# Kernel tuning notes

Measured on AMD Instinct MI355X. Metric: run time of the kernel, lower is better.

The kernel has to match this reference:

```python
import jax, jax.numpy as jnp
import numpy as np
from jax import lax

N = 100000   # num_nodes
E = 1600000  # num_edges (avg degree 16)
F = 128      # num_features
H = 256      # hidden_channels
C = 64       # num_classes
K = 10       # propagation steps
ALPHA = 0.1
BETA = 0.5
THETA = 0.5
EPS = 1e-5   # BatchNorm eps


def setup_inputs() -> dict:
    key = jax.random.key(0)
    ks = jax.random.split(key, 16)
    x = jax.random.normal(ks[0], (N, F), dtype=jnp.float32)
    src = jax.random.randint(ks[1], (E,), 0, N, dtype=jnp.int32)
    dst = jax.random.randint(ks[2], (E,), 0, N, dtype=jnp.int32)
    # row-normalized adjacency weights so repeated A@z stays bounded
    deg = jax.ops.segment_sum(jnp.ones((E,), jnp.float32), dst, num_segments=N)
    w = (1.0 / jnp.maximum(deg, 1.0))[dst]
    # MLP params (Linear + BatchNorm per hidden layer)
    W1 = jax.random.normal(ks[3], (F, H), dtype=jnp.float32) * 0.05
    b1 = jnp.zeros((H,), jnp.float32)
    g1 = jnp.ones((H,), jnp.float32)
    be1 = jnp.zeros((H,), jnp.float32)
    W2 = jax.random.normal(ks[4], (H, H), dtype=jnp.float32) * 0.05
    b2 = jnp.zeros((H,), jnp.float32)
    g2 = jnp.ones((H,), jnp.float32)
    be2 = jnp.zeros((H,), jnp.float32)
    W3 = jax.random.normal(ks[5], (H, C), dtype=jnp.float32) * 0.05
    b3 = jnp.zeros((C,), jnp.float32)
    # lazy caches (warm-start memories); nonzero so the blend branch is taken
    z_sam = jax.random.normal(ks[6], (N, C), dtype=jnp.float32) * 0.1
    g_sam = jax.random.normal(ks[7], (N, C), dtype=jnp.float32) * 0.01
    return dict(x=x, src=src, dst=dst, w=w,
                W1=W1, b1=b1, g1=g1, be1=be1,
                W2=W2, b2=b2, g2=g2, be2=be2,
                W3=W3, b3=b3, z_sam=z_sam, g_sam=g_sam, size=N)


def _bn(h, gamma, beta):
    # BatchNorm1d in training mode: batch statistics over nodes
    mu = jnp.mean(h, axis=0)
    var = jnp.var(h, axis=0)
    return (h - mu) * jax.lax.rsqrt(var + EPS) * gamma + beta


def reference(x, src, dst, w, W1, b1, g1, be1, W2, b2, g2, be2, W3, b3,
              z_sam, g_sam, size):
    # MLP stack: Linear -> BN -> ReLU (dropout omitted: deterministic reference)
    h = jax.nn.relu(_bn(x @ W1 + b1, g1, be1))
    h = jax.nn.relu(_bn(h @ W2 + b2, g2, be2))
    logits = h @ W3 + b3  # [N, C]

    def spmm(z):
        # (A @ z)_i = sum_{j -> i} w_ij * z_j
        return jax.ops.segment_sum(z[src] * w[:, None], dst, num_segments=N)

    # Lazy_Prop.forward: warm-start blend, then K propagation steps
    use_x = jnp.all(z_sam[:size] == 0.0)
    z0 = jnp.where(use_x, logits, (1.0 - BETA) * z_sam + BETA * logits)
    z = lax.fori_loop(0, K, lambda i, z: (1.0 - ALPHA) * spmm(z) + ALPHA * logits, z0)
    return jax.nn.log_softmax(z, axis=1)
```

## Files before the change

kernel.cpp:

```cpp
#include <hip/hip_runtime.h>
#include <hip/hip_bf16.h>

#define NODES 100000
#define EDGES 1600000
#define FEAT  128
#define HID   256
#define CLS   64
#define KPROP 10
#define ALPHA_C 0.1f
#define BETA_C  0.5f
#define BN_EPS  1e-5f

typedef __attribute__((ext_vector_type(8))) short short8;
typedef __attribute__((ext_vector_type(4))) float f32x4;

static __device__ __forceinline__ unsigned short f2b(float f) {
    __hip_bfloat16 h = __float2bfloat16(f);
    return *(unsigned short*)&h;
}
static __device__ __forceinline__ float b2f(unsigned short u) {
    __hip_bfloat16 h;
    *(unsigned short*)&h = u;
    return __bfloat162float(h);
}
static __device__ __forceinline__ float asf(unsigned int u) {
    union { unsigned int u; float f; } c; c.u = u; return c.f;
}

__global__ void packwt_k(const float* __restrict__ W, unsigned short* __restrict__ Wt,
                         int K, int N)
{
    int i = blockIdx.x * 256 + threadIdx.x;
    if (i < K * N) {
        int k = i / N, n = i - k * N;
        Wt[(size_t)n * K + k] = f2b(W[i]);
    }
}

__global__ void xcvt_k(const float* __restrict__ x, unsigned short* __restrict__ xb)
{
    int i = blockIdx.x * 256 + threadIdx.x;
    if (i < NODES * FEAT / 8) {
        float4 a = ((const float4*)x)[2 * i];
        float4 b = ((const float4*)x)[2 * i + 1];
        short8 o;
        o[0] = (short)f2b(a.x); o[1] = (short)f2b(a.y);
        o[2] = (short)f2b(a.z); o[3] = (short)f2b(a.w);
        o[4] = (short)f2b(b.x); o[5] = (short)f2b(b.y);
        o[6] = (short)f2b(b.z); o[7] = (short)f2b(b.w);
        ((short8*)xb)[i] = o;
    }
}

__global__ __launch_bounds__(256, 2)
void gemm1_k(const unsigned short* __restrict__ xb, const unsigned short* __restrict__ Wt,
             const float* __restrict__ bias, unsigned short* __restrict__ h1,
             float* __restrict__ gsum, float* __restrict__ gsq,
             int M, int nchunks, int nblk)
{
    __shared__ unsigned short Blds[256 * FEAT];
    const int lane = threadIdx.x & 63;
    const int wv   = threadIdx.x >> 6;
    const int quad = lane >> 4;
    const int l16  = lane & 15;
    const int colbase = wv * 64;

    #pragma unroll
    for (int i0 = 0; i0 < 4096; i0 += 256) {
        int i  = i0 + threadIdx.x;
        int c  = i >> 4;
        int k8 = i & 15;
        short8 v = *(const short8*)(Wt + (size_t)c * FEAT + k8 * 8);
        int byte = c * 256 + ((k8 * 16) ^ ((c & 7) << 4));
        *(short8*)((char*)Blds + byte) = v;
    }
    __syncthreads();

    float bcol[4];
    #pragma unroll
    for (int ct = 0; ct < 4; ++ct) bcol[ct] = bias[colbase + ct * 16 + l16];
    float ps[4] = {0.f, 0.f, 0.f, 0.f};
    float pq[4] = {0.f, 0.f, 0.f, 0.f};

    short8 ah0[2][4], ah1[2][4];

#define LOAD1(AH, CHK)                                                         \
    if ((CHK) < nchunks) {                                                     \
        const int rb_ = (CHK) * 32;                                            \
        _Pragma("unroll")                                                      \
        for (int rt = 0; rt < 2; ++rt) {                                       \
            const int row_ = rb_ + rt * 16 + l16;                              \
            const bool ok_ = row_ < M;                                         \
            const unsigned short* ap_ = xb + (size_t)row_ * FEAT + quad * 8;   \
            _Pragma("unroll")                                                  \
            for (int ks = 0; ks < 4; ++ks)                                     \
                AH[rt][ks] = ok_ ? *(const short8*)(ap_ + ks * 32)             \
                                 : (short8){0, 0, 0, 0, 0, 0, 0, 0};           \
        }                                                                      \
    }

#define COMP1(AH, CHK)                                                         \
    {                                                                          \
        const int rb_ = (CHK) * 32;                                            \
        f32x4 acc[2][4];                                                       \
        _Pragma("unroll")                                                      \
        for (int i = 0; i < 2; ++i)                                            \
            _Pragma("unroll")                                                  \
            for (int j = 0; j < 4; ++j)                                        \
                acc[i][j] = (f32x4){0.f, 0.f, 0.f, 0.f};                       \
        _Pragma("unroll")                                                      \
        for (int ks = 0; ks < 4; ++ks) {                                       \
            _Pragma("unroll")                                                  \
            for (int ct = 0; ct < 4; ++ct) {                                   \
                const int col_ = colbase + ct * 16 + l16;                      \
                const int boff = col_ * 256                                    \
                               + ((ks * 64 + quad * 16) ^ ((col_ & 7) << 4));  \
                short8 bf = *(const short8*)((const char*)Blds + boff);        \
                acc[0][ct] = __builtin_amdgcn_mfma_f32_16x16x32_bf16(AH[0][ks], bf, acc[0][ct], 0, 0, 0); \
                acc[1][ct] = __builtin_amdgcn_mfma_f32_16x16x32_bf16(AH[1][ks], bf, acc[1][ct], 0, 0, 0); \
            }                                                                  \
        }                                                                      \
        _Pragma("unroll")                                                      \
        for (int ct = 0; ct < 4; ++ct) {                                       \
            const int col_ = colbase + ct * 16 + l16;                          \
            _Pragma("unroll")                                                  \
            for (int rt = 0; rt < 2; ++rt) {                                   \
                _Pragma("unroll")                                              \
                for (int r2 = 0; r2 < 4; ++r2) {                               \
                    const int row_ = rb_ + rt * 16 + quad * 4 + r2;            \
                    if (row_ < M) {                                            \
                        float vv = acc[rt][ct][r2] + bcol[ct];                 \
                        ps[ct] += vv; pq[ct] += vv * vv;                       \
                        h1[(size_t)row_ * HID + col_] = f2b(vv);               \
                    }                                                          \
                }                                                              \
            }                                                                  \
        }                                                                      \
    }

    int chunk = blockIdx.x;
    LOAD1(ah0, chunk)
    while (chunk < nchunks) {
        const int cn1 = chunk + nblk;
        LOAD1(ah1, cn1)
        __builtin_amdgcn_sched_barrier(0);
        COMP1(ah0, chunk)
        chunk = cn1;
        if (chunk >= nchunks) break;
        const int cn2 = chunk + nblk;
        LOAD1(ah0, cn2)
        __builtin_amdgcn_sched_barrier(0);
        COMP1(ah1, chunk)
        chunk = cn2;
    }
#undef LOAD1
#undef COMP1

    #pragma unroll
    for (int ct = 0; ct < 4; ++ct) {
        float s = ps[ct];
        s += __shfl_xor(s, 16, 64);
        s += __shfl_xor(s, 32, 64);
        float q = pq[ct];
        q += __shfl_xor(q, 16, 64);
        q += __shfl_xor(q, 32, 64);
        if (lane < 16) {
            atomicAdd(&gsum[colbase + ct * 16 + lane], s);
            atomicAdd(&gsq[colbase + ct * 16 + lane], q);
        }
    }
}

template<bool AF32, bool FUSE, bool STATS, bool OUTF32, int KK, int NCOLG>
__global__ __launch_bounds__(256, 2)
void gemm_lds_k(const void* __restrict__ Ain, const unsigned short* __restrict__ Wt,
                const float* __restrict__ bias,
                const float* __restrict__ scale, const float* __restrict__ shift,
                void* __restrict__ outp,
                float* __restrict__ gsum, float* __restrict__ gsq,
                int M, int N, int nchunks, int nblk)
{
    constexpr int NK8 = KK / 32;
    __shared__ unsigned short Blds[64 * KK];
    __shared__ float Slds[KK];
    __shared__ float Hlds[KK];

    const int lane = threadIdx.x & 63;
    const int wv   = threadIdx.x >> 6;
    const int quad = lane >> 4;
    const int l16  = lane & 15;
    const int colg = (NCOLG > 1) ? (blockIdx.x % NCOLG) : 0;
    const int blk0 = (NCOLG > 1) ? (blockIdx.x / NCOLG) : blockIdx.x;
    const int colbase = colg * 64;

    {
        const unsigned short* wp = Wt + (size_t)colbase * KK;
        constexpr int ELEMS = 64 * KK / 8;
        #pragma unroll
        for (int i0 = 0; i0 < ELEMS; i0 += 256) {
            int i  = i0 + threadIdx.x;
            int c  = i / (KK / 8);
            int k8 = i - c * (KK / 8);
            short8 v = *(const short8*)(wp + (size_t)c * KK + k8 * 8);
            int byte = c * (KK * 2) + ((k8 * 16) ^ ((c & 7) << 4));
            *(short8*)((char*)Blds + byte) = v;
        }
        if constexpr (FUSE) {
            for (int i = threadIdx.x; i < KK; i += 256) {
                Slds[i] = scale[i];
                Hlds[i] = shift[i];
            }
        }
    }
    __syncthreads();

    float bcol[4];
    #pragma unroll
    for (int ct = 0; ct < 4; ++ct) bcol[ct] = bias[colbase + ct * 16 + l16];

    float ps[4] = {0.f, 0.f, 0.f, 0.f};
    float pq[4] = {0.f, 0.f, 0.f, 0.f};

    float4 af0[2][AF32 ? NK8 : 1][2];
    float4 af1[2][AF32 ? NK8 : 1][2];
    short8 ah0[2][AF32 ? 1 : NK8];
    short8 ah1[2][AF32 ? 1 : NK8];

#define LOAD_A(AF, AH, CHK)                                                    \
    if ((CHK) < nchunks) {                                                     \
        const int rb_ = (CHK) * 128 + wv * 32;                                 \
        _Pragma("unroll")                                                      \
        for (int rt = 0; rt < 2; ++rt) {                                       \
            const int row_ = rb_ + rt * 16 + l16;                              \
            const bool ok_ = row_ < M;                                         \
            if constexpr (AF32) {                                              \
                const float* ap_ = (const float*)Ain + (size_t)row_ * KK + quad * 8; \
                _Pragma("unroll")                                              \
                for (int ks = 0; ks < NK8; ++ks) {                             \
                    AF[rt][ks][0] = ok_ ? *(const float4*)(ap_ + ks * 32)                \
                                        : (float4){0.f, 0.f, 0.f, 0.f};        \
                    AF[rt][ks][1] = ok_ ? *(const float4*)(ap_ + ks * 32 + 4)            \
                                        : (float4){0.f, 0.f, 0.f, 0.f};        \
                }                                                              \
            } else {                                                           \
                const unsigned short* ap_ = (const unsigned short*)Ain + (size_t)row_ * KK + quad * 8; \
                _Pragma("unroll")                                              \
                for (int ks = 0; ks < NK8; ++ks)                               \
                    AH[rt][ks] = ok_ ? *(const short8*)(ap_ + ks * 32)         \
                                     : (short8){0, 0, 0, 0, 0, 0, 0, 0};       \
            }                                                                  \
        }                                                                      \
    }

#define COMPUTE(AF, AH, CHK)                                                   \
    {                                                                          \
        const int rb_ = (CHK) * 128 + wv * 32;                                 \
        f32x4 acc[2][4];                                                       \
        _Pragma("unroll")                                                      \
        for (int i = 0; i < 2; ++i)                                            \
            _Pragma("unroll")                                                  \
            for (int j = 0; j < 4; ++j)                                        \
                acc[i][j] = (f32x4){0.f, 0.f, 0.f, 0.f};                       \
        _Pragma("unroll")                                                      \
        for (int ks = 0; ks < NK8; ++ks) {                                     \
            const int k_ = ks * 32 + quad * 8;                                 \
            float sc[8], sh[8];                                                \
            if constexpr (FUSE) {                                              \
                float4 s0 = *(const float4*)&Slds[k_];                         \
                float4 s1 = *(const float4*)&Slds[k_ + 4];                     \
                float4 h0 = *(const float4*)&Hlds[k_];                         \
                float4 h1 = *(const float4*)&Hlds[k_ + 4];                     \
                sc[0]=s0.x; sc[1]=s0.y; sc[2]=s0.z; sc[3]=s0.w;                \
                sc[4]=s1.x; sc[5]=s1.y; sc[6]=s1.z; sc[7]=s1.w;                \
                sh[0]=h0.x; sh[1]=h0.y; sh[2]=h0.z; sh[3]=h0.w;                \
                sh[4]=h1.x; sh[5]=h1.y; sh[6]=h1.z; sh[7]=h1.w;                \
            }                                                                  \
            short8 a2[2];                                                      \
            _Pragma("unroll")                                                  \
            for (int rt = 0; rt < 2; ++rt) {                                   \
                float v[8];                                                    \
                if constexpr (AF32) {                                          \
                    float4 t0 = AF[rt][ks][0];                                 \
                    float4 t1 = AF[rt][ks][1];                                 \
                    v[0]=t0.x; v[1]=t0.y; v[2]=t0.z; v[3]=t0.w;                \
                    v[4]=t1.x; v[5]=t1.y; v[6]=t1.z; v[7]=t1.w;                \
                } else {                                                       \
                    _Pragma("unroll")                                          \
                    for (int j = 0; j < 8; ++j)                                \
                        v[j] = b2f((unsigned short)AH[rt][ks][j]);             \
                }                                                              \
                if constexpr (FUSE) {                                          \
                    _Pragma("unroll")                                          \
                    for (int j = 0; j < 8; ++j)                                \
                        v[j] = fmaxf(fmaf(v[j], sc[j], sh[j]), 0.f);           \
                }                                                              \
                short8 av;                                                     \
                _Pragma("unroll")                                              \
                for (int j = 0; j < 8; ++j) av[j] = (short)f2b(v[j]);          \
                a2[rt] = av;                                                   \
            }                                                                  \
            _Pragma("unroll")                                                  \
            for (int ct = 0; ct < 4; ++ct) {                                   \
                const int boff = (ct * 16 + l16) * (KK * 2)                    \
                               + ((ks * 64 + quad * 16) ^ ((l16 & 7) << 4));   \
                short8 bf = *(const short8*)((const char*)Blds + boff);        \
                acc[0][ct] = __builtin_amdgcn_mfma_f32_16x16x32_bf16(a2[0], bf, acc[0][ct], 0, 0, 0); \
                acc[1][ct] = __builtin_amdgcn_mfma_f32_16x16x32_bf16(a2[1], bf, acc[1][ct], 0, 0, 0); \
            }                                                                  \
        }                                                                      \
        _Pragma("unroll")                                                      \
        for (int ct = 0; ct < 4; ++ct) {                                       \
            const int col_ = colbase + ct * 16 + l16;                          \
            _Pragma("unroll")                                                  \
            for (int rt = 0; rt < 2; ++rt) {                                   \
                _Pragma("unroll")                                              \
                for (int r2 = 0; r2 < 4; ++r2) {                               \
                    const int row_ = rb_ + rt * 16 + quad * 4 + r2;            \
                    if (row_ < M) {                                            \
                        float vv = acc[rt][ct][r2] + bcol[ct];                 \
                        if constexpr (STATS) { ps[ct] += vv; pq[ct] += vv * vv; } \
                        if constexpr (OUTF32) {                                \
                            ((float*)outp)[(size_t)row_ * N + col_] = vv;      \
                        } else {                                               \
                            ((unsigned short*)outp)[(size_t)row_ * N + col_] = f2b(vv); \
                        }                                                      \
                    }                                                          \
                }                                                              \
            }                                                                  \
        }                                                                      \
    }

    int chunk = blk0;
    LOAD_A(af0, ah0, chunk)
    while (chunk < nchunks) {
        const int cn1 = chunk + nblk;
        LOAD_A(af1, ah1, cn1)
        __builtin_amdgcn_sched_barrier(0);
        COMPUTE(af0, ah0, chunk)
        chunk = cn1;
        if (chunk >= nchunks) break;
        const int cn2 = chunk + nblk;
        LOAD_A(af0, ah0, cn2)
        __builtin_amdgcn_sched_barrier(0);
        COMPUTE(af1, ah1, chunk)
        chunk = cn2;
    }
#undef LOAD_A
#undef COMPUTE

    if constexpr (STATS) {
        #pragma unroll
        for (int ct = 0; ct < 4; ++ct) {
            float s = ps[ct];
            s += __shfl_xor(s, 16, 64);
            s += __shfl_xor(s, 32, 64);
            float q = pq[ct];
            q += __shfl_xor(q, 16, 64);
            q += __shfl_xor(q, 32, 64);
            if (lane < 16) {
                atomicAdd(&gsum[colbase + ct * 16 + lane], s);
                atomicAdd(&gsq[colbase + ct * 16 + lane], q);
            }
        }
    }
}

__global__ void bnfin_k(const float* __restrict__ sum, const float* __restrict__ sq,
                        const float* __restrict__ g, const float* __restrict__ be,
                        float* __restrict__ scale, float* __restrict__ shift)
{
    int c = threadIdx.x;
    float mu = sum[c] * (1.f / NODES);
    float var = sq[c] * (1.f / NODES) - mu * mu;
    float sc = g[c] * rsqrtf(var + BN_EPS);
    scale[c] = sc;
    shift[c] = be[c] - mu * sc;
}

__global__ void flag_k(const float* __restrict__ zs, int* __restrict__ flag)
{
    int i = blockIdx.x * 256 + threadIdx.x;
    bool nz = (i < NODES * CLS) && (zs[i] != 0.f);
    if (__any(nz)) {
        if ((threadIdx.x & 63) == 0) *flag = 1;
    }
}

__global__ void blend_k(const float* __restrict__ zs, const float* __restrict__ logits,
                        const int* __restrict__ flag, unsigned short* __restrict__ z0)
{
    int i = blockIdx.x * 256 + threadIdx.x;
    if (i < NODES * CLS) {
        float l = logits[i];
        float v = (*flag) ? ((1.f - BETA_C) * zs[i] + BETA_C * l) : l;
        int row = i >> 6, c = i & 63, p = c >> 5;
        z0[((size_t)p * NODES + row) * 32 + (c & 31)] = f2b(v);
    }
}

__global__ void count_k(const int* __restrict__ dst, int* __restrict__ cntx)
{
    int t = blockIdx.x * 256 + threadIdx.x;
    if (t >= EDGES / 4) return;
    int4 d = ((const int4*)dst)[t];
    int* c = cntx + (size_t)(blockIdx.x & 7) * NODES;
    atomicAdd(&c[d.x], 1);
    atomicAdd(&c[d.y], 1);
    atomicAdd(&c[d.z], 1);
    atomicAdd(&c[d.w], 1);
}

__global__ void sumoff_k(int* __restrict__ cntx, int* __restrict__ cnt)
{
    int n = blockIdx.x * 256 + threadIdx.x;
    if (n >= NODES) return;
    int tot = 0;
    int p[8];
    #pragma unroll
    for (int x = 0; x < 8; ++x) {
        p[x] = tot;
        tot += cntx[(size_t)x * NODES + n];
    }
    #pragma unroll
    for (int x = 0; x < 8; ++x)
        cntx[(size_t)x * NODES + n] = p[x];
    cnt[n] = tot;
}

__global__ void scan1_k(const int* __restrict__ cnt, int* __restrict__ rowptr,
                        int* __restrict__ bsum)
{
    __shared__ int s[256];
    int tid = threadIdx.x;
    int i = blockIdx.x * 256 + tid;
    int v = (i < NODES) ? cnt[i] : 0;
    s[tid] = v;
    __syncthreads();
    for (int off = 1; off < 256; off <<= 1) {
        int t = (tid >= off) ? s[tid - off] : 0;
        __syncthreads();
        s[tid] += t;
        __syncthreads();
    }
    if (i < NODES) rowptr[i] = s[tid] - v;
    if (tid == 255) bsum[blockIdx.x] = s[255];
}

__global__ void scan2_k(const int* __restrict__ bsum, int* __restrict__ boffs, int nb)
{
    __shared__ int s[512];
    int tid = threadIdx.x;
    int v = (tid < nb) ? bsum[tid] : 0;
    s[tid] = v;
    __syncthreads();
    for (int off = 1; off < 512; off <<= 1) {
        int t = (tid >= off) ? s[tid - off] : 0;
        __syncthreads();
        s[tid] += t;
        __syncthreads();
    }
    if (tid < nb) boffs[tid] = s[tid] - v;
}

__global__ void scan3_k(int* __restrict__ rowptr, const int* __restrict__ boffs,
                        const int* __restrict__ cntx, int* __restrict__ curx)
{
    int i = blockIdx.x * 256 + threadIdx.x;
    if (i < NODES) {
        int v = rowptr[i] + boffs[blockIdx.x];
        rowptr[i] = v;
        #pragma unroll
        for (int x = 0; x < 8; ++x)
            curx[(size_t)x * NODES + i] = v + cntx[(size_t)x * NODES + i];
    }
    if (i == 0) rowptr[NODES] = EDGES;
}

__global__ void posfill_k(const int* __restrict__ dst, int* __restrict__ curx,
                          int* __restrict__ pos)
{
    int t = blockIdx.x * 256 + threadIdx.x;
    if (t >= EDGES / 4) return;
    int4 d = ((const int4*)dst)[t];
    int* cur = curx + (size_t)(blockIdx.x & 7) * NODES;
    int4 p;
    p.x = atomicAdd(&cur[d.x], 1);
    p.y = atomicAdd(&cur[d.y], 1);
    p.z = atomicAdd(&cur[d.z], 1);
    p.w = atomicAdd(&cur[d.w], 1);
    ((int4*)pos)[t] = p;
}

__global__ void scat_k(const int* __restrict__ src, const int* __restrict__ pos,
                       int* __restrict__ esrc)
{
    int e = blockIdx.x * 256 + threadIdx.x;
    if (e < EDGES) esrc[pos[e]] = src[e];
}

__global__ __launch_bounds__(256)
void prop_k(const int* __restrict__ rowptr, const int* __restrict__ esrc,
            const unsigned long long* __restrict__ zin, const float* __restrict__ logits,
            uint4* __restrict__ zout)
{
    const int p = blockIdx.y;
    int row = blockIdx.x * 64 + (threadIdx.x >> 2);
    if (row >= NODES) return;
    int l4 = threadIdx.x & 3;
    int beg = rowptr[row], end = rowptr[row + 1];
    const unsigned long long* zp = zin + (size_t)p * NODES * 8;
    float a0 = 0.f, a1 = 0.f, a2 = 0.f, a3 = 0.f;
    float a4 = 0.f, a5 = 0.f, a6 = 0.f, a7 = 0.f;

    for (int cbeg = beg; cbeg < end; cbeg += 16) {
        int cnt = min(16, end - cbeg);
        int eb = cbeg + l4 * 4;
        int s0 = (eb     < end) ? esrc[eb]     : 0;
        int s1 = (eb + 1 < end) ? esrc[eb + 1] : 0;
        int s2 = (eb + 2 < end) ? esrc[eb + 2] : 0;
        int s3 = (eb + 3 < end) ? esrc[eb + 3] : 0;
        if (cnt == 16) {
            int idx[16];
            #pragma unroll
            for (int j = 0; j < 16; ++j) {
                int sv = (j & 3) == 0 ? s0 : (j & 3) == 1 ? s1 : (j & 3) == 2 ? s2 : s3;
                idx[j] = __shfl(sv, j >> 2, 4);
            }
            unsigned long long vv[32];
            #pragma unroll
            for (int j = 0; j < 16; ++j) {
                const unsigned long long* bp = zp + (size_t)idx[j] * 8 + l4 * 2;
                vv[2 * j]     = __hip_atomic_load(bp,     __ATOMIC_RELAXED, __HIP_MEMORY_SCOPE_AGENT);
                vv[2 * j + 1] = __hip_atomic_load(bp + 1, __ATOMIC_RELAXED, __HIP_MEMORY_SCOPE_AGENT);
            }
            #pragma unroll
            for (int j = 0; j < 16; ++j) {
                unsigned int x0 = (unsigned int)vv[2 * j];
                unsigned int x1 = (unsigned int)(vv[2 * j] >> 32);
                unsigned int x2 = (unsigned int)vv[2 * j + 1];
                unsigned int x3 = (unsigned int)(vv[2 * j + 1] >> 32);
                a0 += asf(x0 << 16);  a1 += asf(x0 & 0xffff0000u);
                a2 += asf(x1 << 16);  a3 += asf(x1 & 0xffff0000u);
                a4 += asf(x2 << 16);  a5 += asf(x2 & 0xffff0000u);
                a6 += asf(x3 << 16);  a7 += asf(x3 & 0xffff0000u);
            }
        } else {
            for (int j = 0; j < cnt; ++j) {
                int sv = (j & 3) == 0 ? s0 : (j & 3) == 1 ? s1 : (j & 3) == 2 ? s2 : s3;
                int id = __shfl(sv, j >> 2, 4);
                const unsigned long long* bp = zp + (size_t)id * 8 + l4 * 2;
                unsigned long long v0 = __hip_atomic_load(bp,     __ATOMIC_RELAXED, __HIP_MEMORY_SCOPE_AGENT);
                unsigned long long v1 = __hip_atomic_load(bp + 1, __ATOMIC_RELAXED, __HIP_MEMORY_SCOPE_AGENT);
                unsigned int x0 = (unsigned int)v0;
                unsigned int x1 = (unsigned int)(v0 >> 32);
                unsigned int x2 = (unsigned int)v1;
                unsigned int x3 = (unsigned int)(v1 >> 32);
                a0 += asf(x0 << 16);  a1 += asf(x0 & 0xffff0000u);
                a2 += asf(x1 << 16);  a3 += asf(x1 & 0xffff0000u);
                a4 += asf(x2 << 16);  a5 += asf(x2 & 0xffff0000u);
                a6 += asf(x3 << 16);  a7 += asf(x3 & 0xffff0000u);
            }
        }
    }
    float dg = (float)(end - beg);
    float inv = 1.f / fmaxf(dg, 1.f);
    float cc = (1.f - ALPHA_C) * inv;
    const float* lp = logits + (size_t)row * CLS + p * 32 + l4 * 8;
    float4 lv0 = *(const float4*)lp;
    float4 lv1 = *(const float4*)(lp + 4);
    float r0 = cc * a0 + ALPHA_C * lv0.x;
    float r1 = cc * a1 + ALPHA_C * lv0.y;
    float r2 = cc * a2 + ALPHA_C * lv0.z;
    float r3 = cc * a3 + ALPHA_C * lv0.w;
    float r4 = cc * a4 + ALPHA_C * lv1.x;
    float r5 = cc * a5 + ALPHA_C * lv1.y;
    float r6 = cc * a6 + ALPHA_C * lv1.z;
    float r7 = cc * a7 + ALPHA_C * lv1.w;
    uint4 w;
    w.x = ((unsigned int)f2b(r1) << 16) | (unsigned int)f2b(r0);
    w.y = ((unsigned int)f2b(r3) << 16) | (unsigned int)f2b(r2);
    w.z = ((unsigned int)f2b(r5) << 16) | (unsigned int)f2b(r4);
    w.w = ((unsigned int)f2b(r7) << 16) | (unsigned int)f2b(r6);
    zout[((size_t)p * NODES + row) * 4 + l4] = w;
}

__global__ __launch_bounds__(256)
void logsoftmax_k(const unsigned short* __restrict__ z, float* __restrict__ out)
{
    int row = blockIdx.x * 4 + (threadIdx.x >> 6);
    if (row >= NODES) return;
    int lane = threadIdx.x & 63;
    int p = lane >> 5;
    float v = b2f(z[((size_t)p * NODES + row) * 32 + (lane & 31)]);
    float m = v;
    #pragma unroll
    for (int off = 32; off > 0; off >>= 1) m = fmaxf(m, __shfl_xor(m, off, 64));
    float ex = expf(v - m);
    float s = ex;
    #pragma unroll
    for (int off = 32; off > 0; off >>= 1) s += __shfl_xor(s, off, 64);
    out[(size_t)row * CLS + lane] = (v - m) - logf(s);
}

extern "C" void kernel_launch(void* const* d_in, const int* in_sizes, int n_in,
                              void* d_out, int out_size, void* d_ws, size_t ws_size,
                              hipStream_t stream)
{
    const float* x   = (const float*)d_in[0];
    const int*   src = (const int*)d_in[1];
    const int*   dst = (const int*)d_in[2];
    const float* W1  = (const float*)d_in[4];
    const float* b1  = (const float*)d_in[5];
    const float* g1  = (const float*)d_in[6];
    const float* be1 = (const float*)d_in[7];
    const float* W2  = (const float*)d_in[8];
    const float* b2  = (const float*)d_in[9];
    const float* g2  = (const float*)d_in[10];
    const float* be2 = (const float*)d_in[11];
    const float* W3  = (const float*)d_in[12];
    const float* b3  = (const float*)d_in[13];
    const float* zsam = (const float*)d_in[14];
    float* outp = (float*)d_out;

    uint8_t* base = (uint8_t*)d_ws;
    float* s_scale1 = (float*)(base);
    float* s_shift1 = s_scale1 + 256;
    float* s_scale2 = s_shift1 + 256;
    float* s_shift2 = s_scale2 + 256;
    float* s_sum    = s_shift2 + 256;
    float* s_sq     = s_sum + 256;
    int*   flag     = (int*)(s_sq + 256);

    unsigned short* Wt1 = (unsigned short*)(base + (1 << 14));
    unsigned short* Wt2 = Wt1 + (size_t)FEAT * HID;
    unsigned short* Wt3 = Wt2 + (size_t)HID * HID;
    unsigned short* h1  = Wt3 + (size_t)HID * CLS;
    unsigned short* h2  = h1 + (size_t)NODES * HID;
    float* logits = (float*)(h2 + (size_t)NODES * HID);
    unsigned short* zA  = (unsigned short*)(logits + (size_t)NODES * CLS);
    unsigned short* zB  = zA + (size_t)NODES * CLS;
    int* esrc   = (int*)(zB + (size_t)NODES * CLS);
    int* cntx   = esrc + EDGES;
    int* curx   = cntx + (size_t)8 * NODES;
    int* rowptr = curx + (size_t)8 * NODES;
    int* cnt    = rowptr + (NODES + 1);
    int* bsum   = cnt + NODES;
    int* boffs  = bsum + 512;
    int* pos = (int*)h1;
    unsigned short* xb = h2;

    const int NCHUNK = (NODES + 127) / 128;
    const int NBLK   = (NCHUNK + 1) / 2;
    const int NCH1   = (NODES + 31) / 32;
    const int NB1    = 512;
    const int SCANB  = (NODES + 255) / 256;
    const int EB4    = (EDGES / 4 + 255) / 256;

    packwt_k<<<(FEAT * HID + 255) / 256, 256, 0, stream>>>(W1, Wt1, FEAT, HID);
    packwt_k<<<(HID * HID + 255) / 256, 256, 0, stream>>>(W2, Wt2, HID, HID);
    packwt_k<<<(HID * CLS + 255) / 256, 256, 0, stream>>>(W3, Wt3, HID, CLS);
    xcvt_k<<<(NODES * FEAT / 8 + 255) / 256, 256, 0, stream>>>(x, xb);

    hipMemsetAsync(cntx, 0, (size_t)8 * NODES * sizeof(int), stream);
    count_k<<<EB4, 256, 0, stream>>>(dst, cntx);
    sumoff_k<<<SCANB, 256, 0, stream>>>(cntx, cnt);
    scan1_k<<<SCANB, 256, 0, stream>>>(cnt, rowptr, bsum);
    scan2_k<<<1, 512, 0, stream>>>(bsum, boffs, SCANB);
    scan3_k<<<SCANB, 256, 0, stream>>>(rowptr, boffs, cntx, curx);
    posfill_k<<<EB4, 256, 0, stream>>>(dst, curx, pos);
    scat_k<<<EDGES / 256, 256, 0, stream>>>(src, pos, esrc);

    hipMemsetAsync(s_sum, 0, 512 * sizeof(float), stream);
    gemm1_k<<<NB1, 256, 0, stream>>>(xb, Wt1, b1, h1, s_sum, s_sq, NODES, NCH1, NB1);
    bnfin_k<<<1, 256, 0, stream>>>(s_sum, s_sq, g1, be1, s_scale1, s_shift1);

    hipMemsetAsync(s_sum, 0, 512 * sizeof(float), stream);
    gemm_lds_k<false, true, true, false, HID, 4><<<NBLK * 4, 256, 0, stream>>>(
        h1, Wt2, b2, s_scale1, s_shift1, h2, s_sum, s_sq, NODES, HID, NCHUNK, NBLK);
    bnfin_k<<<1, 256, 0, stream>>>(s_sum, s_sq, g2, be2, s_scale2, s_shift2);

    gemm_lds_k<false, true, false, true, HID, 1><<<NBLK, 256, 0, stream>>>(
        h2, Wt3, b3, s_scale2, s_shift2, logits, nullptr, nullptr, NODES, CLS, NCHUNK, NBLK);

    hipMemsetAsync(flag, 0, sizeof(int), stream);
    flag_k<<<(NODES * CLS + 255) / 256, 256, 0, stream>>>(zsam, flag);
    blend_k<<<(NODES * CLS + 255) / 256, 256, 0, stream>>>(zsam, logits, flag, zA);

    const dim3 PGRID((NODES + 63) / 64, 2);
    for (int it = 0; it < KPROP; ++it) {
        const unsigned long long* zi = (const unsigned long long*)((it & 1) ? zB : zA);
        uint4* zo = (uint4*)((it & 1) ? zA : zB);
        prop_k<<<PGRID, 256, 0, stream>>>(rowptr, esrc, zi, logits, zo);
    }

    logsoftmax_k<<<(NODES + 3) / 4, 256, 0, stream>>>(zA, outp);
}
```

Measured before the change: 1.013 ms.

## Unsplit propagation layout to full 128B rows and half-K pipeline the GEMM

The propagation state moves from two 32-column planes to a single row-major bf16 layout, so each node row is a full 128-byte line gathered by 8 lanes per row in one launch instead of two grid slices. The intent is fewer edge-index loads and better use of each gathered cache line. The LDS GEMM drops its fp32-A path and double-buffers half-K slices of the A tile inside each chunk, with the accumulator and epilogue hoisted, to cut register pressure. The trade-off is more lanes per row and the loss of some cross-chunk prefetch depth.

```diff
diff --git a/kernel.cpp b/kernel.cpp
--- a/kernel.cpp
+++ b/kernel.cpp
@@ -171,9 +171,9 @@
     }
 }
 
-template<bool AF32, bool FUSE, bool STATS, bool OUTF32, int KK, int NCOLG>
+template<bool FUSE, bool STATS, bool OUTF32, int KK, int NCOLG>
 __global__ __launch_bounds__(256, 2)
-void gemm_lds_k(const void* __restrict__ Ain, const unsigned short* __restrict__ Wt,
+void gemm_lds_k(const unsigned short* __restrict__ Ain, const unsigned short* __restrict__ Wt,
                 const float* __restrict__ bias,
                 const float* __restrict__ scale, const float* __restrict__ shift,
                 void* __restrict__ outp,
@@ -181,6 +181,7 @@
                 int M, int N, int nchunks, int nblk)
 {
     constexpr int NK8 = KK / 32;
+    constexpr int NKH = NK8 / 2;
     __shared__ unsigned short Blds[64 * KK];
     __shared__ float Slds[KK];
     __shared__ float Hlds[KK];
@@ -221,49 +222,31 @@
     float ps[4] = {0.f, 0.f, 0.f, 0.f};
     float pq[4] = {0.f, 0.f, 0.f, 0.f};
 
-    float4 af0[2][AF32 ? NK8 : 1][2];
-    float4 af1[2][AF32 ? NK8 : 1][2];
-    short8 ah0[2][AF32 ? 1 : NK8];
-    short8 ah1[2][AF32 ? 1 : NK8];
-
-#define LOAD_A(AF, AH, CHK)                                                    \
+    short8 hb0[2][NKH], hb1[2][NKH];
+    f32x4 acc[2][4];
+
+#define LOADH(B, CHK, H)                                                       \
     if ((CHK) < nchunks) {                                                     \
         const int rb_ = (CHK) * 128 + wv * 32;                                 \
         _Pragma("unroll")                                                      \
         for (int rt = 0; rt < 2; ++rt) {                                       \
             const int row_ = rb_ + rt * 16 + l16;                              \
             const bool ok_ = row_ < M;                                         \
-            if constexpr (AF32) {                                              \
-                const float* ap_ = (const float*)Ain + (size_t)row_ * KK + quad * 8; \
-                _Pragma("unroll")                                              \
-                for (int ks = 0; ks < NK8; ++ks) {                             \
-                    AF[rt][ks][0] = ok_ ? *(const float4*)(ap_ + ks * 32)                \
-                                        : (float4){0.f, 0.f, 0.f, 0.f};        \
-                    AF[rt][ks][1] = ok_ ? *(const float4*)(ap_ + ks * 32 + 4)            \
-                                        : (float4){0.f, 0.f, 0.f, 0.f};        \
-                }                                                              \
-            } else {                                                           \
-                const unsigned short* ap_ = (const unsigned short*)Ain + (size_t)row_ * KK + quad * 8; \
-                _Pragma("unroll")                                              \
-                for (int ks = 0; ks < NK8; ++ks)                               \
-                    AH[rt][ks] = ok_ ? *(const short8*)(ap_ + ks * 32)         \
-                                     : (short8){0, 0, 0, 0, 0, 0, 0, 0};       \
-            }                                                                  \
+            const unsigned short* ap_ = Ain + (size_t)row_ * KK                \
+                                        + (H) * NKH * 32 + quad * 8;           \
+            _Pragma("unroll")                                                  \
+            for (int ks = 0; ks < NKH; ++ks)                                   \
+                B[rt][ks] = ok_ ? *(const short8*)(ap_ + ks * 32)              \
+                                : (short8){0, 0, 0, 0, 0, 0, 0, 0};            \
         }                                                                      \
     }
 
-#define COMPUTE(AF, AH, CHK)                                                   \
+#define COMPH(B, H)                                                            \
     {                                                                          \
-        const int rb_ = (CHK) * 128 + wv * 32;                                 \
-        f32x4 acc[2][4];                                                       \
         _Pragma("unroll")                                                      \
-        for (int i = 0; i < 2; ++i)                                            \
-            _Pragma("unroll")                                                  \
-            for (int j = 0; j < 4; ++j)                                        \
-                acc[i][j] = (f32x4){0.f, 0.f, 0.f, 0.f};                       \
-        _Pragma("unroll")                                                      \
-        for (int ks = 0; ks < NK8; ++ks) {                                     \
-            const int k_ = ks * 32 + quad * 8;                                 \
+        for (int ks = 0; ks < NKH; ++ks) {                                     \
+            const int gks = (H) * NKH + ks;                                    \
+            const int k_ = gks * 32 + quad * 8;                                \
             float sc[8], sh[8];                                                \
             if constexpr (FUSE) {                                              \
                 float4 s0 = *(const float4*)&Slds[k_];                         \
@@ -278,75 +261,75 @@
             short8 a2[2];                                                      \
             _Pragma("unroll")                                                  \
             for (int rt = 0; rt < 2; ++rt) {                                   \
-                float v[8];                                                    \
-                if constexpr (AF32) {                                          \
-                    float4 t0 = AF[rt][ks][0];                                 \
-                    float4 t1 = AF[rt][ks][1];                                 \
-                    v[0]=t0.x; v[1]=t0.y; v[2]=t0.z; v[3]=t0.w;                \
-                    v[4]=t1.x; v[5]=t1.y; v[6]=t1.z; v[7]=t1.w;                \
-                } else {                                                       \
+                if constexpr (FUSE) {                                          \
+                    float v[8];                                                \
                     _Pragma("unroll")                                          \
                     for (int j = 0; j < 8; ++j)                                \
-                        v[j] = b2f((unsigned short)AH[rt][ks][j]);             \
-                }                                                              \
-                if constexpr (FUSE) {                                          \
+                        v[j] = b2f((unsigned short)B[rt][ks][j]);              \
                     _Pragma("unroll")                                          \
                     for (int j = 0; j < 8; ++j)                                \
                         v[j] = fmaxf(fmaf(v[j], sc[j], sh[j]), 0.f);           \
+                    short8 av;                                                 \
+                    _Pragma("unroll")                                          \
+                    for (int j = 0; j < 8; ++j) av[j] = (short)f2b(v[j]);      \
+                    a2[rt] = av;                                               \
+                } else {                                                       \
+                    a2[rt] = B[rt][ks];                                        \
                 }                                                              \
-                short8 av;                                                     \
-                _Pragma("unroll")                                              \
-                for (int j = 0; j < 8; ++j) av[j] = (short)f2b(v[j]);          \
-                a2[rt] = av;                                                   \
             }                                                                  \
             _Pragma("unroll")                                                  \
             for (int ct = 0; ct < 4; ++ct) {                                   \
                 const int boff = (ct * 16 + l16) * (KK * 2)                    \
-                               + ((ks * 64 + quad * 16) ^ ((l16 & 7) << 4));   \
+                               + ((gks * 64 + quad * 16) ^ ((l16 & 7) << 4));  \
                 short8 bf = *(const short8*)((const char*)Blds + boff);        \
                 acc[0][ct] = __builtin_amdgcn_mfma_f32_16x16x32_bf16(a2[0], bf, acc[0][ct], 0, 0, 0); \
                 acc[1][ct] = __builtin_amdgcn_mfma_f32_16x16x32_bf16(a2[1], bf, acc[1][ct], 0, 0, 0); \
             }                                                                  \
         }                                                                      \
-        _Pragma("unroll")                                                      \
-        for (int ct = 0; ct < 4; ++ct) {                                       \
-            const int col_ = colbase + ct * 16 + l16;                          \
-            _Pragma("unroll")                                                  \
-            for (int rt = 0; rt < 2; ++rt) {                                   \
-                _Pragma("unroll")                                              \
-                for (int r2 = 0; r2 < 4; ++r2) {                               \
-                    const int row_ = rb_ + rt * 16 + quad * 4 + r2;            \
-                    if (row_ < M) {                                            \
-                        float vv = acc[rt][ct][r2] + bcol[ct];                 \
-                        if constexpr (STATS) { ps[ct] += vv; pq[ct] += vv * vv; } \
-                        if constexpr (OUTF32) {                                \
-                            ((float*)outp)[(size_t)row_ * N + col_] = vv;      \
-                        } else {                                               \
-                            ((unsigned short*)outp)[(size_t)row_ * N + col_] = f2b(vv); \
-                        }                                                      \
-                    }                                                          \
-                }                                                              \
-            }                                                                  \
-        }                                                                      \
     }
 
     int chunk = blk0;
-    LOAD_A(af0, ah0, chunk)
+    LOADH(hb0, chunk, 0)
     while (chunk < nchunks) {
-        const int cn1 = chunk + nblk;
-        LOAD_A(af1, ah1, cn1)
+        #pragma unroll
+        for (int i = 0; i < 2; ++i)
+            #pragma unroll
+            for (int j = 0; j < 4; ++j)
+                acc[i][j] = (f32x4){0.f, 0.f, 0.f, 0.f};
+
+        LOADH(hb1, chunk, 1)
         __builtin_amdgcn_sched_barrier(0);
-        COMPUTE(af0, ah0, chunk)
-        chunk = cn1;
-        if (chunk >= nchunks) break;
-        const int cn2 = chunk + nblk;
-        LOAD_A(af0, ah0, cn2)
+        COMPH(hb0, 0)
+        const int nxt = chunk + nblk;
+        LOADH(hb0, nxt, 0)
         __builtin_amdgcn_sched_barrier(0);
-        COMPUTE(af1, ah1, chunk)
-        chunk = cn2;
-    }
-#undef LOAD_A
-#undef COMPUTE
+        COMPH(hb1, 1)
+
+        const int rb_ = chunk * 128 + wv * 32;
+        #pragma unroll
+        for (int ct = 0; ct < 4; ++ct) {
+            const int col_ = colbase + ct * 16 + l16;
+            #pragma unroll
+            for (int rt = 0; rt < 2; ++rt) {
+                #pragma unroll
+                for (int r2 = 0; r2 < 4; ++r2) {
+                    const int row_ = rb_ + rt * 16 + quad * 4 + r2;
+                    if (row_ < M) {
+                        float vv = acc[rt][ct][r2] + bcol[ct];
+                        if constexpr (STATS) { ps[ct] += vv; pq[ct] += vv * vv; }
+                        if constexpr (OUTF32) {
+                            ((float*)outp)[(size_t)row_ * N + col_] = vv;
+                        } else {
+                            ((unsigned short*)outp)[(size_t)row_ * N + col_] = f2b(vv);
+                        }
+                    }
+                }
+            }
+        }
+        chunk = nxt;
+    }
+#undef LOADH
+#undef COMPH
 
     if constexpr (STATS) {
         #pragma unroll
@@ -393,8 +376,7 @@
     if (i < NODES * CLS) {
         float l = logits[i];
         float v = (*flag) ? ((1.f - BETA_C) * zs[i] + BETA_C * l) : l;
-        int row = i >> 6, c = i & 63, p = c >> 5;
-        z0[((size_t)p * NODES + row) * 32 + (c & 31)] = f2b(v);
+        z0[i] = f2b(v);
     }
 }
 
@@ -503,42 +485,37 @@
             const unsigned long long* __restrict__ zin, const float* __restrict__ logits,
             uint4* __restrict__ zout)
 {
-    const int p = blockIdx.y;
-    int row = blockIdx.x * 64 + (threadIdx.x >> 2);
+    int row = blockIdx.x * 32 + (threadIdx.x >> 3);
     if (row >= NODES) return;
-    int l4 = threadIdx.x & 3;
+    int l8 = threadIdx.x & 7;
     int beg = rowptr[row], end = rowptr[row + 1];
-    const unsigned long long* zp = zin + (size_t)p * NODES * 8;
     float a0 = 0.f, a1 = 0.f, a2 = 0.f, a3 = 0.f;
     float a4 = 0.f, a5 = 0.f, a6 = 0.f, a7 = 0.f;
 
     for (int cbeg = beg; cbeg < end; cbeg += 16) {
+        int e0 = cbeg + l8, e1 = cbeg + 8 + l8;
+        int s0 = (e0 < end) ? esrc[e0] : 0;
+        int s1 = (e1 < end) ? esrc[e1] : 0;
         int cnt = min(16, end - cbeg);
-        int eb = cbeg + l4 * 4;
-        int s0 = (eb     < end) ? esrc[eb]     : 0;
-        int s1 = (eb + 1 < end) ? esrc[eb + 1] : 0;
-        int s2 = (eb + 2 < end) ? esrc[eb + 2] : 0;
-        int s3 = (eb + 3 < end) ? esrc[eb + 3] : 0;
         if (cnt == 16) {
             int idx[16];
             #pragma unroll
-            for (int j = 0; j < 16; ++j) {
-                int sv = (j & 3) == 0 ? s0 : (j & 3) == 1 ? s1 : (j & 3) == 2 ? s2 : s3;
-                idx[j] = __shfl(sv, j >> 2, 4);
-            }
+            for (int u = 0; u < 8; ++u) idx[u] = __shfl(s0, u, 8);
+            #pragma unroll
+            for (int u = 0; u < 8; ++u) idx[8 + u] = __shfl(s1, u, 8);
             unsigned long long vv[32];
             #pragma unroll
-            for (int j = 0; j < 16; ++j) {
-                const unsigned long long* bp = zp + (size_t)idx[j] * 8 + l4 * 2;
-                vv[2 * j]     = __hip_atomic_load(bp,     __ATOMIC_RELAXED, __HIP_MEMORY_SCOPE_AGENT);
-                vv[2 * j + 1] = __hip_atomic_load(bp + 1, __ATOMIC_RELAXED, __HIP_MEMORY_SCOPE_AGENT);
+            for (int u = 0; u < 16; ++u) {
+                const unsigned long long* p = zin + (size_t)idx[u] * 16 + l8 * 2;
+                vv[2 * u]     = __hip_atomic_load(p,     __ATOMIC_RELAXED, __HIP_MEMORY_SCOPE_AGENT);
+                vv[2 * u + 1] = __hip_atomic_load(p + 1, __ATOMIC_RELAXED, __HIP_MEMORY_SCOPE_AGENT);
             }
             #pragma unroll
-            for (int j = 0; j < 16; ++j) {
-                unsigned int x0 = (unsigned int)vv[2 * j];
-                unsigned int x1 = (unsigned int)(vv[2 * j] >> 32);
-                unsigned int x2 = (unsigned int)vv[2 * j + 1];
-                unsigned int x3 = (unsigned int)(vv[2 * j + 1] >> 32);
+            for (int u = 0; u < 16; ++u) {
+                unsigned int x0 = (unsigned int)vv[2 * u];
+                unsigned int x1 = (unsigned int)(vv[2 * u] >> 32);
+                unsigned int x2 = (unsigned int)vv[2 * u + 1];
+                unsigned int x3 = (unsigned int)(vv[2 * u + 1] >> 32);
                 a0 += asf(x0 << 16);  a1 += asf(x0 & 0xffff0000u);
                 a2 += asf(x1 << 16);  a3 += asf(x1 & 0xffff0000u);
                 a4 += asf(x2 << 16);  a5 += asf(x2 & 0xffff0000u);
@@ -546,11 +523,10 @@
             }
         } else {
             for (int j = 0; j < cnt; ++j) {
-                int sv = (j & 3) == 0 ? s0 : (j & 3) == 1 ? s1 : (j & 3) == 2 ? s2 : s3;
-                int id = __shfl(sv, j >> 2, 4);
-                const unsigned long long* bp = zp + (size_t)id * 8 + l4 * 2;
-                unsigned long long v0 = __hip_atomic_load(bp,     __ATOMIC_RELAXED, __HIP_MEMORY_SCOPE_AGENT);
-                unsigned long long v1 = __hip_atomic_load(bp + 1, __ATOMIC_RELAXED, __HIP_MEMORY_SCOPE_AGENT);
+                int sv = (j < 8) ? __shfl(s0, j, 8) : __shfl(s1, j - 8, 8);
+                const unsigned long long* p = zin + (size_t)sv * 16 + l8 * 2;
+                unsigned long long v0 = __hip_atomic_load(p,     __ATOMIC_RELAXED, __HIP_MEMORY_SCOPE_AGENT);
+                unsigned long long v1 = __hip_atomic_load(p + 1, __ATOMIC_RELAXED, __HIP_MEMORY_SCOPE_AGENT);
                 unsigned int x0 = (unsigned int)v0;
                 unsigned int x1 = (unsigned int)(v0 >> 32);
                 unsigned int x2 = (unsigned int)v1;
@@ -565,7 +541,7 @@
     float dg = (float)(end - beg);
     float inv = 1.f / fmaxf(dg, 1.f);
     float cc = (1.f - ALPHA_C) * inv;
-    const float* lp = logits + (size_t)row * CLS + p * 32 + l4 * 8;
+    const float* lp = logits + (size_t)row * CLS + l8 * 8;
     float4 lv0 = *(const float4*)lp;
     float4 lv1 = *(const float4*)(lp + 4);
     float r0 = cc * a0 + ALPHA_C * lv0.x;
@@ -581,7 +557,7 @@
     w.y = ((unsigned int)f2b(r3) << 16) | (unsigned int)f2b(r2);
     w.z = ((unsigned int)f2b(r5) << 16) | (unsigned int)f2b(r4);
     w.w = ((unsigned int)f2b(r7) << 16) | (unsigned int)f2b(r6);
-    zout[((size_t)p * NODES + row) * 4 + l4] = w;
+    zout[(size_t)row * 8 + l8] = w;
 }
 
 __global__ __launch_bounds__(256)
@@ -590,8 +566,7 @@
     int row = blockIdx.x * 4 + (threadIdx.x >> 6);
     if (row >= NODES) return;
     int lane = threadIdx.x & 63;
-    int p = lane >> 5;
-    float v = b2f(z[((size_t)p * NODES + row) * 32 + (lane & 31)]);
+    float v = b2f(z[(size_t)row * CLS + lane]);
     float m = v;
     #pragma unroll
     for (int off = 32; off > 0; off >>= 1) m = fmaxf(m, __shfl_xor(m, off, 64));
@@ -675,22 +650,22 @@
     bnfin_k<<<1, 256, 0, stream>>>(s_sum, s_sq, g1, be1, s_scale1, s_shift1);
 
     hipMemsetAsync(s_sum, 0, 512 * sizeof(float), stream);
-    gemm_lds_k<false, true, true, false, HID, 4><<<NBLK * 4, 256, 0, stream>>>(
+    gemm_lds_k<true, true, false, HID, 4><<<NBLK * 4, 256, 0, stream>>>(
         h1, Wt2, b2, s_scale1, s_shift1, h2, s_sum, s_sq, NODES, HID, NCHUNK, NBLK);
     bnfin_k<<<1, 256, 0, stream>>>(s_sum, s_sq, g2, be2, s_scale2, s_shift2);
 
-    gemm_lds_k<false, true, false, true, HID, 1><<<NBLK, 256, 0, stream>>>(
+    gemm_lds_k<true, false, true, HID, 1><<<NBLK, 256, 0, stream>>>(
         h2, Wt3, b3, s_scale2, s_shift2, logits, nullptr, nullptr, NODES, CLS, NCHUNK, NBLK);
 
     hipMemsetAsync(flag, 0, sizeof(int), stream);
     flag_k<<<(NODES * CLS + 255) / 256, 256, 0, stream>>>(zsam, flag);
     blend_k<<<(NODES * CLS + 255) / 256, 256, 0, stream>>>(zsam, logits, flag, zA);
 
-    const dim3 PGRID((NODES + 63) / 64, 2);
+    const int PROPB = (NODES + 31) / 32;
     for (int it = 0; it < KPROP; ++it) {
         const unsigned long long* zi = (const unsigned long long*)((it & 1) ? zB : zA);
         uint4* zo = (uint4*)((it & 1) ? zA : zB);
-        prop_k<<<PGRID, 256, 0, stream>>>(rowptr, esrc, zi, logits, zo);
+        prop_k<<<PROPB, 256, 0, stream>>>(rowptr, esrc, zi, logits, zo);
     }
 
     logsoftmax_k<<<(NODES + 3) / 4, 256, 0, stream>>>(zA, outp);
```

Result: faster. 866.3 us (-14.5%).
